# Kernel tuning notes

Measured on AMD Instinct MI355X. Metric: run time of the kernel, lower is better.

## Reference

```python
import jax, jax.numpy as jnp
import numpy as np

RADIUS = 0.1
NSAMPLE = 32


def setup_inputs() -> dict:
    key = jax.random.key(0)
    k1, k2, k3 = jax.random.split(key, 3)
    B, N, P, C = 2, 16384, 4096, 64
    xyz = jax.random.uniform(k1, (B, N, 3), dtype=jnp.float32)
    new_xyz = jax.random.uniform(k2, (B, P, 3), dtype=jnp.float32)
    features = jax.random.normal(k3, (B, C, N), dtype=jnp.float32)
    return {"xyz": xyz, "new_xyz": new_xyz, "features": features}


def _ball_query(xyz, new_xyz, radius, nsample):
    """Return (B, npoint, nsample) int32 indices of the first `nsample` points
    (in original order) within `radius` of each query center. Slots beyond the
    number of valid neighbors are padded with the first valid index (0 if none),
    matching the standard PointNet++ CUDA ball_query semantics."""
    N = xyz.shape[1]
    # squared distances [B, P, N]
    d2 = jnp.sum((new_xyz[:, :, None, :] - xyz[:, None, :, :]) ** 2, axis=-1)
    in_ball = d2 < (radius * radius)
    # score = point index if in ball, else N (sentinel); smallest nsample scores
    # are the first nsample in-ball indices in original order.
    score = jnp.where(in_ball, jnp.arange(N, dtype=jnp.int32), jnp.int32(N))
    neg_topk, _ = jax.lax.top_k(-score, nsample)  # largest of -score == smallest score
    idx = -neg_topk  # [B, P, nsample], ascending
    first = idx[..., :1]
    idx = jnp.where(idx >= N, first, idx)  # pad invalid slots with first valid
    idx = jnp.where(idx >= N, 0, idx)      # no neighbor at all -> 0
    return idx


def _group(features, idx):
    """features (B, C, N), idx (B, P, S) -> (B, C, P, S)"""
    return jax.vmap(lambda f, i: f[:, i])(features, idx)


def reference(xyz, new_xyz, features):
    idx = _ball_query(xyz, new_xyz, RADIUS, NSAMPLE)          # (B, P, S)
    xyz_t = jnp.transpose(xyz, (0, 2, 1))                      # (B, 3, N)
    grouped_xyz = _group(xyz_t, idx)                           # (B, 3, P, S)
    grouped_xyz = grouped_xyz - jnp.transpose(new_xyz, (0, 2, 1))[..., None]
    grouped_features = _group(features, idx)                   # (B, C, P, S)
    new_features = jnp.concatenate([grouped_xyz, grouped_features], axis=1)
    return new_features
```

## Files before the change

### kernel.cpp

```cpp
#include <hip/hip_runtime.h>
#include <limits.h>

#define BB 2
#define NN 16384
#define PP 4096
#define CC 64
#define SS 32
#define R2 0.01f
#define OUTCH (3 + CC)

__global__ __launch_bounds__(256) void ball_query_kernel(
    const float* __restrict__ xyz, const float* __restrict__ new_xyz,
    int* __restrict__ idx_out) {
#pragma clang fp contract(off)
  const int wave = blockIdx.x * 4 + (threadIdx.x >> 6);
  const int lane = threadIdx.x & 63;
  const int b = wave >> 12;

  const float cx = new_xyz[wave * 3 + 0];
  const float cy = new_xyz[wave * 3 + 1];
  const float cz = new_xyz[wave * 3 + 2];
  const float4* __restrict__ xb4 = (const float4*)(xyz + (size_t)b * NN * 3);
  int* __restrict__ myout = idx_out + wave * SS;

  const unsigned long long below = (1ull << lane) - 1ull;

  int cnt = 0;
  int firstCand = INT_MAX;

  for (int chunk = 0; chunk < NN; chunk += 256) {
    const int q0 = chunk + 4 * lane;
    const float4* pf = xb4 + 3 * (size_t)(q0 >> 2);
    const float4 f0 = pf[0];
    const float4 f1 = pf[1];
    const float4 f2 = pf[2];

    float dx, dy, dz, a, d2;
    dx = cx - f0.x; dy = cy - f0.y; dz = cz - f0.z;
    a = dx * dx + dy * dy; d2 = a + dz * dz;
    const bool c0 = d2 < R2;
    dx = cx - f0.w; dy = cy - f1.x; dz = cz - f1.y;
    a = dx * dx + dy * dy; d2 = a + dz * dz;
    const bool c1 = d2 < R2;
    dx = cx - f1.z; dy = cy - f1.w; dz = cz - f2.x;
    a = dx * dx + dy * dy; d2 = a + dz * dz;
    const bool c2 = d2 < R2;
    dx = cx - f2.y; dy = cy - f2.z; dz = cz - f2.w;
    a = dx * dx + dy * dy; d2 = a + dz * dz;
    const bool c3 = d2 < R2;

    const unsigned long long b0 = __ballot(c0);
    const unsigned long long b1 = __ballot(c1);
    const unsigned long long b2 = __ballot(c2);
    const unsigned long long b3 = __ballot(c3);

    const int m = (c0 ? 1 : 0) | (c1 ? 2 : 0) | (c2 ? 4 : 0) | (c3 ? 8 : 0);

    if (m) {
      const int pre = (int)__popcll(b0 & below) + (int)__popcll(b1 & below) +
                      (int)__popcll(b2 & below) + (int)__popcll(b3 & below);
      firstCand = min(firstCand, q0 + __builtin_ctz(m));
      int s = cnt + pre;
      if (m & 1) { if (s < SS) myout[s] = q0 + 0; ++s; }
      if (m & 2) { if (s < SS) myout[s] = q0 + 1; ++s; }
      if (m & 4) { if (s < SS) myout[s] = q0 + 2; ++s; }
      if (m & 8) { if (s < SS) myout[s] = q0 + 3; }
    }

    cnt += (int)__popcll(b0) + (int)__popcll(b1) + (int)__popcll(b2) +
           (int)__popcll(b3);
    if (cnt >= SS) break;
  }

  int fc = firstCand;
#pragma unroll
  for (int d = 32; d; d >>= 1) fc = min(fc, __shfl_xor(fc, d));
  if (fc == INT_MAX) fc = 0;

  for (int s = cnt + lane; s < SS; s += 64) myout[s] = fc;
}

__global__ __launch_bounds__(256) void transpose_feat_kernel(
    const float* __restrict__ feat, float* __restrict__ featT) {
  __shared__ float tile[64][65];
  const int n0 = blockIdx.x * 64;
  const int b = blockIdx.y;
  const int jn = threadIdx.x & 63;
  const int g4 = threadIdx.x >> 6;

  const float* fb = feat + (size_t)b * CC * NN;
#pragma unroll
  for (int k = 0; k < 16; ++k) {
    const int c = g4 * 16 + k;
    tile[c][jn] = fb[(size_t)c * NN + n0 + jn];
  }
  __syncthreads();
  float* ft = featT + ((size_t)b * NN + n0) * CC;
#pragma unroll
  for (int k = 0; k < 16; ++k) {
    const int j = g4 * 16 + k;
    ft[(size_t)j * CC + jn] = tile[jn][j];
  }
}

#define TILE 128
__global__ __launch_bounds__(256) void group_kernel_t(
    const float* __restrict__ xyz, const float* __restrict__ new_xyz,
    const float* __restrict__ featT, const int* __restrict__ idx,
    float* __restrict__ out) {
  __shared__ float lds[TILE * 65];
  const int base = blockIdx.x * TILE;
  const int b = base >> 17;
  const int t = threadIdx.x;
  const size_t PS = (size_t)PP * SS;

  const float4* ftb = (const float4*)(featT + (size_t)b * NN * CC);
#pragma unroll
  for (int k = 0; k < 8; ++k) {
    const int u = k * 256 + t;
    const int r = u >> 4;
    const int q = u & 15;
    const int v = idx[base + r];
    const float4 val = ftb[(size_t)v * 16 + q];
    float* dst = &lds[r * 65 + q * 4];
    dst[0] = val.x; dst[1] = val.y; dst[2] = val.z; dst[3] = val.w;
  }
  __syncthreads();

  if (t < TILE) {
    const int g = base + t;
    const int v = idx[g];
    const int p = (g >> 5) & (PP - 1);
    const float* xr = xyz + ((size_t)b * NN + v) * 3;
    const float* cr = new_xyz + (size_t)(b * PP + p) * 3;
    const size_t ob = (size_t)b * OUTCH * PS + ((size_t)g & (PS - 1));
    out[ob + 0 * PS] = xr[0] - cr[0];
    out[ob + 1 * PS] = xr[1] - cr[1];
    out[ob + 2 * PS] = xr[2] - cr[2];
  }

  float* ob3 = out + (size_t)b * OUTCH * PS + 3 * PS + ((size_t)base & (PS - 1));
#pragma unroll
  for (int k = 0; k < 32; ++k) {
    const int u = k * 256 + t;
    const int c = u >> 7;
    const int r = u & 127;
    ob3[(size_t)c * PS + r] = lds[r * 65 + c];
  }
}

extern "C" void kernel_launch(void* const* d_in, const int* in_sizes, int n_in,
                              void* d_out, int out_size, void* d_ws, size_t ws_size,
                              hipStream_t stream) {
  const float* xyz = (const float*)d_in[0];
  const float* new_xyz = (const float*)d_in[1];
  const float* feat = (const float*)d_in[2];
  float* out = (float*)d_out;

  int* idx = (int*)d_ws;
  const size_t idxBytes = (size_t)BB * PP * SS * sizeof(int);
  float* featT = (float*)((char*)d_ws + idxBytes);

  ball_query_kernel<<<(BB * PP) / 4, 256, 0, stream>>>(xyz, new_xyz, idx);

  transpose_feat_kernel<<<dim3(NN / 64, BB), 256, 0, stream>>>(feat, featT);
  group_kernel_t<<<(BB * PP * SS) / TILE, 256, 0, stream>>>(xyz, new_xyz, featT,
                                                            idx, out);
}
```

Baseline: 71.50 us.

## Replace brute-force ball query with uniform-grid spatial binning and LDS bitmap

Points are binned into a 10x10x10 uniform grid: a histogram pass, a prefix-sum scan and an atomic scatter into cell-sorted float4s that carry the original index. Each query wave then visits only the neighbouring cells and sets bits in a per-wave LDS bitmap of in-ball original indices. A wave-level scan over the bitmap recovers the first 32 neighbours in original order. This removes the long linear scan over up to 16K points per query, at the cost of four extra small kernel launches, global atomics and LDS bitmap clearing.

Result: faster. 62.64 us (-12.4%).

```diff
diff --git a/kernel.cpp b/kernel.cpp
--- a/kernel.cpp
+++ b/kernel.cpp
@@ -8,76 +8,154 @@
 #define SS 32
 #define R2 0.01f
 #define OUTCH (3 + CC)
-
-__global__ __launch_bounds__(256) void ball_query_kernel(
-    const float* __restrict__ xyz, const float* __restrict__ new_xyz,
-    int* __restrict__ idx_out) {
+#define GRES 10
+#define NCELL 1000
+
+__device__ __forceinline__ int cell_of(float v) {
+  int q = (int)(v * 10.0f);
+  return q < 0 ? 0 : (q > GRES - 1 ? GRES - 1 : q);
+}
+__device__ __forceinline__ int cell_clamp_floor(float v) {
+  int q = (int)floorf(v * 10.0f);
+  return q < 0 ? 0 : (q > GRES - 1 ? GRES - 1 : q);
+}
+
+__global__ void zero_counters_kernel(int* hist, int* fill) {
+  const int t = blockIdx.x * blockDim.x + threadIdx.x;
+  if (t < BB * NCELL) { hist[t] = 0; fill[t] = 0; }
+}
+
+__global__ __launch_bounds__(256) void hist_kernel(const float* __restrict__ xyz,
+                                                   int* __restrict__ hist) {
+  const int i = blockIdx.x * 256 + threadIdx.x;
+  const int b = i >> 14;
+  const float* p = xyz + (size_t)i * 3;
+  const int c = (cell_of(p[2]) * GRES + cell_of(p[1])) * GRES + cell_of(p[0]);
+  atomicAdd(hist + b * NCELL + c, 1);
+}
+
+__global__ __launch_bounds__(1024) void scan_kernel(const int* __restrict__ hist,
+                                                    int* __restrict__ cellStart) {
+  __shared__ int sm[1024];
+  const int b = blockIdx.x;
+  const int t = threadIdx.x;
+  const int own = (t < NCELL) ? hist[b * NCELL + t] : 0;
+  sm[t] = own;
+  __syncthreads();
+  for (int off = 1; off < 1024; off <<= 1) {
+    const int v = (t >= off) ? sm[t - off] : 0;
+    __syncthreads();
+    sm[t] += v;
+    __syncthreads();
+  }
+  if (t < NCELL) cellStart[b * 1001 + t] = sm[t] - own;
+  if (t == NCELL - 1) cellStart[b * 1001 + NCELL] = sm[t];
+}
+
+__global__ __launch_bounds__(256) void scatter_kernel(
+    const float* __restrict__ xyz, const int* __restrict__ cellStart,
+    int* __restrict__ fill, float4* __restrict__ sorted4) {
+  const int i = blockIdx.x * 256 + threadIdx.x;
+  const int b = i >> 14;
+  const float* p = xyz + (size_t)i * 3;
+  const float x = p[0], y = p[1], z = p[2];
+  const int c = (cell_of(z) * GRES + cell_of(y)) * GRES + cell_of(x);
+  const int r = atomicAdd(fill + b * NCELL + c, 1);
+  const int pos = cellStart[b * 1001 + c] + r;
+  float4 v;
+  v.x = x; v.y = y; v.z = z; v.w = __int_as_float(i & (NN - 1));
+  sorted4[(size_t)b * NN + pos] = v;
+}
+
+__global__ __launch_bounds__(256) void ball_query_grid(
+    const float4* __restrict__ sorted4, const int* __restrict__ cellStart,
+    const float* __restrict__ new_xyz, int* __restrict__ idx_out) {
 #pragma clang fp contract(off)
-  const int wave = blockIdx.x * 4 + (threadIdx.x >> 6);
+  __shared__ unsigned bmAll[4 * 576];
+  const int widx = threadIdx.x >> 6;
   const int lane = threadIdx.x & 63;
+  const int wave = blockIdx.x * 4 + widx;
   const int b = wave >> 12;
+  unsigned* bm = bmAll + widx * 576;
 
   const float cx = new_xyz[wave * 3 + 0];
   const float cy = new_xyz[wave * 3 + 1];
   const float cz = new_xyz[wave * 3 + 2];
-  const float4* __restrict__ xb4 = (const float4*)(xyz + (size_t)b * NN * 3);
+  const float4* __restrict__ sb = sorted4 + (size_t)b * NN;
+  const int* __restrict__ csb = cellStart + b * 1001;
   int* __restrict__ myout = idx_out + wave * SS;
 
-  const unsigned long long below = (1ull << lane) - 1ull;
-
-  int cnt = 0;
-  int firstCand = INT_MAX;
-
-  for (int chunk = 0; chunk < NN; chunk += 256) {
-    const int q0 = chunk + 4 * lane;
-    const float4* pf = xb4 + 3 * (size_t)(q0 >> 2);
-    const float4 f0 = pf[0];
-    const float4 f1 = pf[1];
-    const float4 f2 = pf[2];
-
-    float dx, dy, dz, a, d2;
-    dx = cx - f0.x; dy = cy - f0.y; dz = cz - f0.z;
-    a = dx * dx + dy * dy; d2 = a + dz * dz;
-    const bool c0 = d2 < R2;
-    dx = cx - f0.w; dy = cy - f1.x; dz = cz - f1.y;
-    a = dx * dx + dy * dy; d2 = a + dz * dz;
-    const bool c1 = d2 < R2;
-    dx = cx - f1.z; dy = cy - f1.w; dz = cz - f2.x;
-    a = dx * dx + dy * dy; d2 = a + dz * dz;
-    const bool c2 = d2 < R2;
-    dx = cx - f2.y; dy = cy - f2.z; dz = cz - f2.w;
-    a = dx * dx + dy * dy; d2 = a + dz * dz;
-    const bool c3 = d2 < R2;
-
-    const unsigned long long b0 = __ballot(c0);
-    const unsigned long long b1 = __ballot(c1);
-    const unsigned long long b2 = __ballot(c2);
-    const unsigned long long b3 = __ballot(c3);
-
-    const int m = (c0 ? 1 : 0) | (c1 ? 2 : 0) | (c2 ? 4 : 0) | (c3 ? 8 : 0);
-
-    if (m) {
-      const int pre = (int)__popcll(b0 & below) + (int)__popcll(b1 & below) +
-                      (int)__popcll(b2 & below) + (int)__popcll(b3 & below);
-      firstCand = min(firstCand, q0 + __builtin_ctz(m));
-      int s = cnt + pre;
-      if (m & 1) { if (s < SS) myout[s] = q0 + 0; ++s; }
-      if (m & 2) { if (s < SS) myout[s] = q0 + 1; ++s; }
-      if (m & 4) { if (s < SS) myout[s] = q0 + 2; ++s; }
-      if (m & 8) { if (s < SS) myout[s] = q0 + 3; }
+#pragma unroll
+  for (int k = 0; k < 9; ++k) bm[k * 64 + lane] = 0;
+
+  const float mg = 0.1f + 1e-5f;
+  const int lox = cell_clamp_floor(cx - mg), hix = cell_clamp_floor(cx + mg);
+  const int loy = cell_clamp_floor(cy - mg), hiy = cell_clamp_floor(cy + mg);
+  const int loz = cell_clamp_floor(cz - mg), hiz = cell_clamp_floor(cz + mg);
+  const int nx = hix - lox + 1;
+
+  for (int zc = loz; zc <= hiz; ++zc) {
+    for (int yc = loy; yc <= hiy; ++yc) {
+      const int c0 = (zc * GRES + yc) * GRES + lox;
+      int s0 = __builtin_amdgcn_readfirstlane(csb[c0]);
+      int e0 = __builtin_amdgcn_readfirstlane(csb[c0 + nx]);
+      for (int o = s0; o < e0; o += 64) {
+        const int j = o + lane;
+        if (j < e0) {
+          const float4 pt = sb[j];
+          const float dx = cx - pt.x;
+          const float dy = cy - pt.y;
+          const float dz = cz - pt.z;
+          const float a = dx * dx + dy * dy;
+          const float d2 = a + dz * dz;
+          if (d2 < R2) {
+            const int orig = __float_as_int(pt.w);
+            const int wi = orig >> 5;
+            atomicOr(&bm[(wi >> 3) * 9 + (wi & 7)], 1u << (orig & 31));
+          }
+        }
+      }
     }
-
-    cnt += (int)__popcll(b0) + (int)__popcll(b1) + (int)__popcll(b2) +
-           (int)__popcll(b3);
-    if (cnt >= SS) break;
-  }
-
-  int fc = firstCand;
-#pragma unroll
-  for (int d = 32; d; d >>= 1) fc = min(fc, __shfl_xor(fc, d));
-  if (fc == INT_MAX) fc = 0;
-
-  for (int s = cnt + lane; s < SS; s += 64) myout[s] = fc;
+  }
+  __threadfence_block();
+
+  unsigned w[8];
+  int c = 0;
+  int fi = INT_MAX;
+#pragma unroll
+  for (int k = 0; k < 8; ++k) {
+    w[k] = bm[lane * 9 + k];
+    c += (int)__popc(w[k]);
+    if (fi == INT_MAX && w[k]) fi = lane * 256 + k * 32 + (int)__builtin_ctz(w[k]);
+  }
+
+  int incl = c;
+#pragma unroll
+  for (int d = 1; d < 64; d <<= 1) {
+    const int t = __shfl_up(incl, d);
+    if (lane >= d) incl += t;
+  }
+  const int E = incl - c;
+  const int total = __shfl(incl, 63);
+
+  const unsigned long long nb = __ballot(c > 0);
+  int fc = 0;
+  if (nb) fc = __shfl(fi, (int)__builtin_ctzll(nb));
+
+  int s = E;
+  if (s < SS) {
+#pragma unroll
+    for (int k = 0; k < 8; ++k) {
+      unsigned ww = w[k];
+      while (ww && s < SS) {
+        const int bpos = (int)__builtin_ctz(ww);
+        ww &= ww - 1;
+        myout[s++] = lane * 256 + k * 32 + bpos;
+      }
+      if (s >= SS) break;
+    }
+  }
+  for (int s2 = total + lane; s2 < SS; s2 += 64) myout[s2] = fc;
 }
 
 __global__ __launch_bounds__(256) void transpose_feat_kernel(
@@ -157,11 +235,20 @@
   const float* feat = (const float*)d_in[2];
   float* out = (float*)d_out;
 
+  const size_t idxBytes = (size_t)BB * PP * SS * sizeof(int);
   int* idx = (int*)d_ws;
-  const size_t idxBytes = (size_t)BB * PP * SS * sizeof(int);
-  float* featT = (float*)((char*)d_ws + idxBytes);
-
-  ball_query_kernel<<<(BB * PP) / 4, 256, 0, stream>>>(xyz, new_xyz, idx);
+  char* ovl = (char*)d_ws + idxBytes;
+  float* featT = (float*)ovl;
+  float4* sorted4 = (float4*)ovl;
+  int* cellStart = (int*)(ovl + (size_t)BB * NN * sizeof(float4));
+  int* hist = cellStart + BB * 1001 + 2;
+  int* fill = hist + BB * NCELL;
+
+  zero_counters_kernel<<<(BB * NCELL + 255) / 256, 256, 0, stream>>>(hist, fill);
+  hist_kernel<<<(BB * NN) / 256, 256, 0, stream>>>(xyz, hist);
+  scan_kernel<<<BB, 1024, 0, stream>>>(hist, cellStart);
+  scatter_kernel<<<(BB * NN) / 256, 256, 0, stream>>>(xyz, cellStart, fill, sorted4);
+  ball_query_grid<<<(BB * PP) / 4, 256, 0, stream>>>(sorted4, cellStart, new_xyz, idx);
 
   transpose_feat_kernel<<<dim3(NN / 64, BB), 256, 0, stream>>>(feat, featT);
   group_kernel_t<<<(BB * PP * SS) / TILE, 256, 0, stream>>>(xyz, new_xyz, featT,
```
